# Optimization experiments

Measured on AMD Instinct MI355X. Metric: run time of the kernel, lower is better.

The kernel has to match this reference:

```python
import jax, jax.numpy as jnp
import numpy as np

EMB_DIM = 1024
HEAD_SIZE = 64
B, T = 4, 4096


def setup_inputs() -> dict:
    key = jax.random.key(0)
    kx, kq, kk, kv = jax.random.split(key, 4)
    scale = 1.0 / np.sqrt(EMB_DIM)
    x = jax.random.normal(kx, (B, T, EMB_DIM), dtype=jnp.float32)
    # weights stored as [emb_dim, head_size] so projection is x @ W
    Wq = jax.random.normal(kq, (EMB_DIM, HEAD_SIZE), dtype=jnp.float32) * scale
    Wk = jax.random.normal(kk, (EMB_DIM, HEAD_SIZE), dtype=jnp.float32) * scale
    Wv = jax.random.normal(kv, (EMB_DIM, HEAD_SIZE), dtype=jnp.float32) * scale
    return {"x": x, "Wq": Wq, "Wk": Wk, "Wv": Wv}


def reference(x, Wq, Wk, Wv):
    # Single causal self-attention head. NOTE: original scales by emb_dim**-0.5
    # (d = x.shape[-1]), not head_size**-0.5 — we reproduce that faithfully.
    _, t, d = x.shape
    q = jnp.einsum('bte,eh->bth', x, Wq)
    k = jnp.einsum('bte,eh->bth', x, Wk)
    v = jnp.einsum('bte,eh->bth', x, Wv)
    wei = jnp.einsum('bth,bsh->bts', q, k) * (d ** -0.5)  # [B, T, T]
    causal = jnp.tril(jnp.ones((t, t), dtype=bool))
    wei = jnp.where(causal, wei, -jnp.inf)
    attn = jax.nn.softmax(wei, axis=-1)
    out = jnp.einsum('bts,bsh->bth', attn, v)  # [B, T, head_size]
    return out
```

## Files before the change

kernel.cpp:

```cpp
#include <hip/hip_runtime.h>
#include <hip/hip_bf16.h>

#define EMB   1024
#define HS    64
#define BATCH 4
#define SEQ   4096
#define MTOT  (BATCH*SEQ)

typedef float  f32x4 __attribute__((ext_vector_type(4)));
typedef short  s16x8 __attribute__((ext_vector_type(8)));
typedef __bf16 bf16x8 __attribute__((ext_vector_type(8)));

__device__ __forceinline__ unsigned short f2bf(float f) {
    unsigned int u = __float_as_uint(f);
    u = (u + 0x7fffu + ((u >> 16) & 1u)) >> 16;
    return (unsigned short)u;
}
__device__ __forceinline__ unsigned int pkbf(float lo, float hi) {
#if __has_builtin(__builtin_amdgcn_cvt_pk_bf16_f32)
    return __builtin_bit_cast(unsigned int,
        __builtin_amdgcn_cvt_pk_bf16_f32(lo, hi));
#else
    return (unsigned int)f2bf(lo) | ((unsigned int)f2bf(hi) << 16);
#endif
}
__device__ __forceinline__ s16x8 cvt8(float4 a, float4 b) {
    union { unsigned int u[4]; s16x8 v; } r;
    r.u[0] = pkbf(a.x, a.y); r.u[1] = pkbf(a.z, a.w);
    r.u[2] = pkbf(b.x, b.y); r.u[3] = pkbf(b.z, b.w);
    return r.v;
}
__device__ __forceinline__ f32x4 mfma16(s16x8 a, s16x8 b, f32x4 c) {
    return __builtin_amdgcn_mfma_f32_16x16x32_bf16(
        __builtin_bit_cast(bf16x8, a), __builtin_bit_cast(bf16x8, b), c, 0, 0, 0);
}
__device__ __forceinline__ void ld_lds16(const void* g, unsigned short* l) {
    __builtin_amdgcn_global_load_lds(
        (const __attribute__((address_space(1))) unsigned int*)g,
        (__attribute__((address_space(3))) unsigned int*)l, 16, 0, 0);
}

__global__ __launch_bounds__(256) void pack_w(const float* __restrict__ Wq,
                                              const float* __restrict__ Wk,
                                              const float* __restrict__ Wv,
                                              unsigned short* __restrict__ wp) {
    int idx = blockIdx.x * 256 + threadIdx.x;
    int l = idx & 63;
    int s = (idx >> 6) & 31;
    int t = idx >> 11;
    const float* W = (t < 4) ? Wq : (t < 8) ? Wk : Wv;
    float scale = (t < 4) ? 0.03125f : 1.0f;
    int n  = ((t & 3) * 16) + (l & 15);
    int k0 = s * 32 + ((l >> 4) * 8);
    s16x8 v;
#pragma unroll
    for (int j = 0; j < 8; j++)
        v[j] = (short)f2bf(W[(size_t)(k0 + j) * HS + n] * scale);
    *(s16x8*)(wp + (size_t)idx * 8) = v;
}

__global__ __launch_bounds__(256) void proj(const float* __restrict__ x,
                                            const unsigned short* __restrict__ wp,
                                            unsigned short* __restrict__ qws,
                                            unsigned short* __restrict__ kws,
                                            unsigned short* __restrict__ vtws) {
    __shared__ unsigned short xb[2][2048];
    __shared__ unsigned short wb[2][6144];
    __shared__ unsigned short vt[32][72];
    int l = threadIdx.x & 63, w = threadIdx.x >> 6;
    int lane15 = l & 15, quad = l >> 4;
    int rh = w & 1, ts = w >> 1;
    int row0 = blockIdx.x * 32;

    auto stage = [&](int buf, int sg) {
        int d = w * 64 + l;
        int row = d >> 3, cs = d & 7;
        int sc = cs ^ (row & 7);
        ld_lds16(x + (size_t)(row0 + row) * EMB + sg * 32 + sc * 4,
                 &xb[buf][w * 512]);
#pragma unroll
        for (int j = 0; j < 3; j++) {
            int f = w + 4 * j;
            ld_lds16(wp + ((size_t)(f * 32 + sg) * 64 + l) * 8,
                     &wb[buf][f * 512]);
        }
    };

    int xrow = rh * 16 + lane15;
    int rsw = xrow & 7;
    f32x4 acc[6] = {};

    stage(0, 0);
    int buf = 0;
    for (int sg = 0; sg < 32; sg++) {
        __syncthreads();
        if (sg < 31) stage(buf ^ 1, sg + 1);

        float4 lo = *(const float4*)&xb[buf][(xrow * 8 + ((2 * quad)     ^ rsw)) * 8];
        float4 hi = *(const float4*)&xb[buf][(xrow * 8 + ((2 * quad + 1) ^ rsw)) * 8];
        s16x8 af = cvt8(lo, hi);
#pragma unroll
        for (int j = 0; j < 6; j++) {
            int t = ts + 2 * j;
            s16x8 bfr = *(const s16x8*)&wb[buf][t * 512 + l * 8];
            acc[j] = mfma16(af, bfr, acc[j]);
        }
        buf ^= 1;
    }

#pragma unroll
    for (int r = 0; r < 4; r++) {
        int row = row0 + rh * 16 + quad * 4 + r;
#pragma unroll
        for (int j = 0; j < 2; j++) {
            int tq = ts + 2 * j;
            int tk = ts + 2 * j + 4;
            int tv = ts + 2 * j + 8;
            qws[(size_t)row * HS + tq * 16 + lane15] = f2bf(acc[j][r]);
            kws[(size_t)row * HS + (tk - 4) * 16 + lane15] = f2bf(acc[j + 2][r]);
            vt[rh * 16 + quad * 4 + r][(tv - 8) * 16 + lane15] = f2bf(acc[j + 4][r]);
        }
    }
    __syncthreads();
    if (threadIdx.x < 128) {
        int h = threadIdx.x & 63, half = threadIdx.x >> 6;
        int b = row0 >> 12, tp0 = row0 & (SEQ - 1);
        unsigned short tmp[16];
#pragma unroll
        for (int j = 0; j < 16; j++) tmp[j] = vt[half * 16 + j][h];
        unsigned short* dst = vtws + ((size_t)b * HS + h) * SEQ + tp0 + half * 16;
        *(s16x8*)dst       = *(s16x8*)tmp;
        *(s16x8*)(dst + 8) = *(s16x8*)(tmp + 8);
    }
}

__global__ __launch_bounds__(256) void attn_part(const unsigned short* __restrict__ qws,
                                                 const unsigned short* __restrict__ kws,
                                                 const unsigned short* __restrict__ vtws,
                                                 float* __restrict__ op,
                                                 float* __restrict__ lp) {
    __shared__ unsigned short ldsK[2][4096];
    __shared__ unsigned short ldsV[2][4096];
    __shared__ unsigned short plds[4][16][72];

    int l = threadIdx.x & 63;
    int w = threadIdx.x >> 6;
    int lane15 = l & 15, quad = l >> 4;

    int W = blockIdx.x;
    int b = W / 288;
    int g = W - b * 288;
    int n = 1;
    while (g >= 4 * n * (n + 1)) n++;
    int off = g - 4 * n * (n - 1);
    int oQ  = (unsigned)off / (unsigned)n;
    int Q   = 8 * (n - 1) + oQ;
    int c   = off - oQ * n;
    int lenT = Q + 1;
    int t0 = c * 8;
    int t1 = min(t0 + 8, lenT);
    int q0 = Q * 64 + w * 16;
    int diag = lenT - 1;

    auto stage = [&](int buf, int c0) {
#pragma unroll
        for (int j = 0; j < 2; j++) {
            int s = w + j * 4;
            int t = s >> 1, h = s & 1;
            ld_lds16(kws + ((size_t)b * SEQ + c0 + t * 16 + lane15) * HS
                         + h * 32 + quad * 8,
                     &ldsK[buf][s * 512]);
            ld_lds16(vtws + ((size_t)b * HS + t * 16 + lane15) * SEQ
                          + c0 + h * 32 + quad * 8,
                     &ldsV[buf][s * 512]);
        }
    };

    const unsigned short* qbase =
        qws + ((size_t)b * SEQ + q0 + lane15) * HS + quad * 8;
    s16x8 qf0 = *(const s16x8*)(qbase);
    s16x8 qf1 = *(const s16x8*)(qbase + 32);

    f32x4 o[4] = {};
    float lsum[4] = {0.f, 0.f, 0.f, 0.f};

    stage(0, t0 * 64);
    int buf = 0;
    for (int kt = t0; kt < t1; kt++) {
        __syncthreads();
        if (kt + 1 < t1) stage(buf ^ 1, (kt + 1) * 64);

        f32x4 sacc[4] = {};
#pragma unroll
        for (int t = 0; t < 4; t++) {
            s16x8 kf0 = *(const s16x8*)(&ldsK[buf][(2 * t) * 512 + l * 8]);
            s16x8 kf1 = *(const s16x8*)(&ldsK[buf][(2 * t + 1) * 512 + l * 8]);
            sacc[t] = mfma16(qf0, kf0, sacc[t]);
            sacc[t] = mfma16(qf1, kf1, sacc[t]);
        }

        if (kt == diag) {
            int c0 = kt * 64;
#pragma unroll
            for (int t = 0; t < 4; t++)
#pragma unroll
                for (int r = 0; r < 4; r++) {
                    int qrow = q0 + quad * 4 + r;
                    int kcol = c0 + t * 16 + lane15;
                    if (kcol > qrow) sacc[t][r] = -1e30f;
                }
        }

#pragma unroll
        for (int t = 0; t < 4; t++)
#pragma unroll
            for (int r = 0; r < 4; r++) {
                float p = __expf(sacc[t][r]);
                lsum[r] += p;
                plds[w][quad * 4 + r][t * 16 + lane15] = f2bf(p);
            }
        __builtin_amdgcn_s_waitcnt(0xC07F);

#pragma unroll
        for (int c2 = 0; c2 < 2; c2++) {
            s16x8 pf = *(const s16x8*)(&plds[w][lane15][c2 * 32 + quad * 8]);
#pragma unroll
            for (int t = 0; t < 4; t++) {
                s16x8 vf = *(const s16x8*)(&ldsV[buf][(2 * t + c2) * 512 + l * 8]);
                o[t] = mfma16(pf, vf, o[t]);
            }
        }
        buf ^= 1;
    }

#pragma unroll
    for (int r = 0; r < 4; r++) {
#pragma unroll
        for (int d = 1; d < 16; d <<= 1)
            lsum[r] += __shfl_xor(lsum[r], d, 64);
    }

    size_t slot = (size_t)b * 288 + g;
    float* ob = op + slot * 4096;
#pragma unroll
    for (int t = 0; t < 4; t++)
#pragma unroll
        for (int r = 0; r < 4; r++)
            ob[(w * 16 + quad * 4 + r) * 64 + t * 16 + lane15] = o[t][r];
    if (lane15 == 0) {
#pragma unroll
        for (int r = 0; r < 4; r++)
            lp[slot * 64 + w * 16 + quad * 4 + r] = lsum[r];
    }
}

__global__ __launch_bounds__(256) void attn_combine(const float* __restrict__ op,
                                                    const float* __restrict__ lp,
                                                    float* __restrict__ out) {
    int e = blockIdx.x * 256 + threadIdx.x;
    int c4 = (e & 15) * 4;
    int row = e >> 4;
    int b   = row >> 12;
    int tr  = row & (SEQ - 1);
    int Q   = tr >> 6;
    int r64 = tr & 63;
    int n   = (Q >> 3) + 1;
    int g0  = 4 * n * (n - 1) + (Q - 8 * (n - 1)) * n;
    f32x4 os = {0.f, 0.f, 0.f, 0.f};
    float ls = 0.f;
    for (int c = 0; c < n; c++) {
        size_t slot = (size_t)b * 288 + g0 + c;
        os += *(const f32x4*)(op + slot * 4096 + r64 * 64 + c4);
        ls += lp[slot * 64 + r64];
    }
    f32x4 r = os / ls;
    *(f32x4*)(out + (size_t)row * HS + c4) = r;
}

extern "C" void kernel_launch(void* const* d_in, const int* in_sizes, int n_in,
                              void* d_out, int out_size, void* d_ws, size_t ws_size,
                              hipStream_t stream) {
    const float* x  = (const float*)d_in[0];
    const float* Wq = (const float*)d_in[1];
    const float* Wk = (const float*)d_in[2];
    const float* Wv = (const float*)d_in[3];
    float* out = (float*)d_out;

    unsigned short* ws   = (unsigned short*)d_ws;
    unsigned short* wp   = ws;
    unsigned short* qws  = ws + 262144;
    unsigned short* kws  = ws + 1310720;
    unsigned short* vtws = ws + 2359296;
    float* op = (float*)(ws + 3407872);
    float* lp = op + 4718592;

    hipLaunchKernelGGL(pack_w,      dim3(96),   dim3(256), 0, stream, Wq, Wk, Wv, wp);
    hipLaunchKernelGGL(proj,        dim3(512),  dim3(256), 0, stream, x, wp, qws, kws, vtws);
    hipLaunchKernelGGL(attn_part,   dim3(1152), dim3(256), 0, stream, qws, kws, vtws, op, lp);
    hipLaunchKernelGGL(attn_combine,dim3(1024), dim3(256), 0, stream, op, lp, out);
}
```

Before: 158.6 us.

## Triple-buffer LDS staging with explicit vmcnt waits in projection and attention

Both the projection and the attention kernels move from double to triple LDS buffers and prefetch two stages ahead. The full __syncthreads is replaced by explicit lgkmcnt(0) and vmcnt(4) waits plus a raw s_barrier, so one stage of async loads can stay in flight across the barrier. Out-of-range prefetches are clamped to the last valid stage, which adds redundant loads and more LDS use, possibly lowering occupancy. Correctness depends on the vmcnt(4) count matching the number of loads per stage.

```diff
diff --git a/kernel.cpp b/kernel.cpp
--- a/kernel.cpp
+++ b/kernel.cpp
@@ -6,6 +6,10 @@
 #define BATCH 4
 #define SEQ   4096
 #define MTOT  (BATCH*SEQ)
+
+#define WAIT_LGKM0() asm volatile("s_waitcnt lgkmcnt(0)" ::: "memory")
+#define WAIT_VM4()   asm volatile("s_waitcnt vmcnt(4)"   ::: "memory")
+#define BAR()        asm volatile("s_barrier"            ::: "memory")
 
 typedef float  f32x4 __attribute__((ext_vector_type(4)));
 typedef short  s16x8 __attribute__((ext_vector_type(8)));
@@ -64,8 +68,8 @@
                                             unsigned short* __restrict__ qws,
                                             unsigned short* __restrict__ kws,
                                             unsigned short* __restrict__ vtws) {
-    __shared__ unsigned short xb[2][2048];
-    __shared__ unsigned short wb[2][6144];
+    __shared__ unsigned short xb[3][2048];
+    __shared__ unsigned short wb[3][6144];
     __shared__ unsigned short vt[32][72];
     int l = threadIdx.x & 63, w = threadIdx.x >> 6;
     int lane15 = l & 15, quad = l >> 4;
@@ -91,11 +95,13 @@
     f32x4 acc[6] = {};
 
     stage(0, 0);
-    int buf = 0;
+    stage(1, 1);
     for (int sg = 0; sg < 32; sg++) {
-        __syncthreads();
-        if (sg < 31) stage(buf ^ 1, sg + 1);
-
+        WAIT_LGKM0();
+        WAIT_VM4();
+        BAR();
+        stage((sg + 2) % 3, min(sg + 2, 31));
+        int buf = sg % 3;
         float4 lo = *(const float4*)&xb[buf][(xrow * 8 + ((2 * quad)     ^ rsw)) * 8];
         float4 hi = *(const float4*)&xb[buf][(xrow * 8 + ((2 * quad + 1) ^ rsw)) * 8];
         s16x8 af = cvt8(lo, hi);
@@ -105,7 +111,6 @@
             s16x8 bfr = *(const s16x8*)&wb[buf][t * 512 + l * 8];
             acc[j] = mfma16(af, bfr, acc[j]);
         }
-        buf ^= 1;
     }
 
 #pragma unroll
@@ -114,11 +119,9 @@
 #pragma unroll
         for (int j = 0; j < 2; j++) {
             int tq = ts + 2 * j;
-            int tk = ts + 2 * j + 4;
-            int tv = ts + 2 * j + 8;
             qws[(size_t)row * HS + tq * 16 + lane15] = f2bf(acc[j][r]);
-            kws[(size_t)row * HS + (tk - 4) * 16 + lane15] = f2bf(acc[j + 2][r]);
-            vt[rh * 16 + quad * 4 + r][(tv - 8) * 16 + lane15] = f2bf(acc[j + 4][r]);
+            kws[(size_t)row * HS + tq * 16 + lane15] = f2bf(acc[j + 2][r]);
+            vt[rh * 16 + quad * 4 + r][tq * 16 + lane15] = f2bf(acc[j + 4][r]);
         }
     }
     __syncthreads();
@@ -139,8 +142,8 @@
                                                  const unsigned short* __restrict__ vtws,
                                                  float* __restrict__ op,
                                                  float* __restrict__ lp) {
-    __shared__ unsigned short ldsK[2][4096];
-    __shared__ unsigned short ldsV[2][4096];
+    __shared__ unsigned short ldsK[3][4096];
+    __shared__ unsigned short ldsV[3][4096];
     __shared__ unsigned short plds[4][16][72];
 
     int l = threadIdx.x & 63;
@@ -162,7 +165,8 @@
     int q0 = Q * 64 + w * 16;
     int diag = lenT - 1;
 
-    auto stage = [&](int buf, int c0) {
+    auto stage = [&](int buf, int kt) {
+        int c0 = min(kt, t1 - 1) * 64;
 #pragma unroll
         for (int j = 0; j < 2; j++) {
             int s = w + j * 4;
@@ -184,11 +188,14 @@
     f32x4 o[4] = {};
     float lsum[4] = {0.f, 0.f, 0.f, 0.f};
 
-    stage(0, t0 * 64);
-    int buf = 0;
+    stage(0, t0);
+    stage(1, t0 + 1);
     for (int kt = t0; kt < t1; kt++) {
-        __syncthreads();
-        if (kt + 1 < t1) stage(buf ^ 1, (kt + 1) * 64);
+        WAIT_LGKM0();
+        WAIT_VM4();
+        BAR();
+        stage((kt - t0 + 2) % 3, kt + 2);
+        int buf = (kt - t0) % 3;
 
         f32x4 sacc[4] = {};
 #pragma unroll
@@ -198,7 +205,6 @@
             sacc[t] = mfma16(qf0, kf0, sacc[t]);
             sacc[t] = mfma16(qf1, kf1, sacc[t]);
         }
-
         if (kt == diag) {
             int c0 = kt * 64;
 #pragma unroll
@@ -210,7 +216,6 @@
                     if (kcol > qrow) sacc[t][r] = -1e30f;
                 }
         }
-
 #pragma unroll
         for (int t = 0; t < 4; t++)
 #pragma unroll
@@ -219,8 +224,7 @@
                 lsum[r] += p;
                 plds[w][quad * 4 + r][t * 16 + lane15] = f2bf(p);
             }
-        __builtin_amdgcn_s_waitcnt(0xC07F);
-
+        WAIT_LGKM0();
 #pragma unroll
         for (int c2 = 0; c2 < 2; c2++) {
             s16x8 pf = *(const s16x8*)(&plds[w][lane15][c2 * 32 + quad * 8]);
@@ -230,7 +234,6 @@
                 o[t] = mfma16(pf, vf, o[t]);
             }
         }
-        buf ^= 1;
     }
 
 #pragma unroll
```

New measurement: 173.8 us. 9.6% more time.
